# Performance work log

Hardware: AMD Instinct MI355X
Metric: run time of the kernel (lower is better)

The kernel has to match this reference:

```python
import jax, jax.numpy as jnp
import numpy as np
import math

B, S, D, H, DH = 1, 2048, 2048, 16, 64  # batch, seq, d_model, n_heads, d_head
LAMBDA_INIT = 0.8
EPS = 1e-5


def setup_inputs() -> dict:
    key = jax.random.key(0)
    ks = jax.random.split(key, 10)
    w_scale = 0.02
    inner = 2 * DH * H  # == D here
    return {
        "x": jax.random.normal(ks[0], (B, S, D), dtype=jnp.float32),
        "Wq": jax.random.normal(ks[1], (D, inner), dtype=jnp.float32) * w_scale,
        "Wk": jax.random.normal(ks[2], (D, inner), dtype=jnp.float32) * w_scale,
        "Wv": jax.random.normal(ks[3], (D, inner), dtype=jnp.float32) * w_scale,
        "Wo": jax.random.normal(ks[4], (inner, D), dtype=jnp.float32) * w_scale,
        "lambda_q1": jax.random.normal(ks[5], (DH,), dtype=jnp.float32) * 0.1,
        "lambda_k1": jax.random.normal(ks[6], (DH,), dtype=jnp.float32) * 0.1,
        "lambda_q2": jax.random.normal(ks[7], (DH,), dtype=jnp.float32) * 0.1,
        "lambda_k2": jax.random.normal(ks[8], (DH,), dtype=jnp.float32) * 0.1,
        "gn_weight": jnp.ones((inner,), dtype=jnp.float32),
        "gn_bias": jnp.zeros((inner,), dtype=jnp.float32),
    }


def reference(x, Wq, Wk, Wv, Wo, lambda_q1, lambda_k1, lambda_q2, lambda_k2,
              gn_weight, gn_bias):
    b, s, _ = x.shape
    dh = lambda_q1.shape[0]
    h = Wq.shape[1] // (2 * dh)
    scale = 1.0 / math.sqrt(dh)

    q = (x @ Wq).reshape(b, s, h, 2, dh)
    k = (x @ Wk).reshape(b, s, h, 2, dh)
    v = (x @ Wv).reshape(b, s, h, 2 * dh)

    # [B,H,S,dh]
    q1 = jnp.swapaxes(q[..., 0, :], 1, 2)
    q2 = jnp.swapaxes(q[..., 1, :], 1, 2)
    k1 = jnp.swapaxes(k[..., 0, :], 1, 2)
    k2 = jnp.swapaxes(k[..., 1, :], 1, 2)
    vh = jnp.swapaxes(v, 1, 2)  # [B,H,S,2*dh]

    score1 = jnp.einsum("bhsd,bhtd->bhst", q1, k1) * scale
    score2 = jnp.einsum("bhsd,bhtd->bhst", q2, k2) * scale
    attn1 = jax.nn.softmax(score1, axis=-1)
    attn2 = jax.nn.softmax(score2, axis=-1)

    lam = (jnp.exp(jnp.sum(lambda_q1 * lambda_k1))
           - jnp.exp(jnp.sum(lambda_q2 * lambda_k2)) + LAMBDA_INIT)

    out = jnp.einsum("bhst,bhtd->bhsd", attn1 - lam * attn2, vh)  # [B,H,S,2dh]
    out = jnp.swapaxes(out, 1, 2)  # [B,S,H,2dh]

    # GroupNorm: n_heads groups over the channel dim, per token
    mu = jnp.mean(out, axis=-1, keepdims=True)
    var = jnp.var(out, axis=-1, keepdims=True)
    out = (out - mu) * jax.lax.rsqrt(var + EPS)
    gw = gn_weight.reshape(h, 2 * dh)
    gb = gn_bias.reshape(h, 2 * dh)
    out = out * gw + gb

    out = out * (1.0 - LAMBDA_INIT)
    return out.reshape(b, s, -1) @ Wo
```

## Files before the change

### kernel.cpp

```cpp
#include <hip/hip_runtime.h>
#include <hip/hip_bf16.h>

typedef unsigned short u16;
typedef __attribute__((ext_vector_type(8))) short short8;
typedef __attribute__((ext_vector_type(4))) short short4v;
typedef __attribute__((ext_vector_type(4))) float f32x4;

#define S_DIM 2048
#define D_DIM 2048
#define H_NUM 16
#define DH_NUM 64

__device__ __forceinline__ u16 f2bf(float f) {
    union { float f; unsigned u; } x; x.f = f;
    unsigned r = x.u + 0x7fff + ((x.u >> 16) & 1);
    return (u16)(r >> 16);
}

__device__ __forceinline__ void gload16(const void* g, void* l) {
    __builtin_amdgcn_global_load_lds(
        (const __attribute__((address_space(1))) unsigned int*)g,
        (__attribute__((address_space(3))) unsigned int*)l, 16, 0, 0);
}

__device__ __forceinline__ void transpose_body(const float* __restrict__ src,
                                               u16* __restrict__ dst,
                                               int tx, int ty, int t)
{
    __shared__ float tile[64][65];
    const int r0 = ty * 64, c0 = tx * 64;
#pragma unroll
    for (int p = 0; p < 4; ++p) {
        int r = p * 16 + (t >> 4), c = (t & 15) * 4;
        float4 v = *(const float4*)&src[(long)(r0 + r) * D_DIM + c0 + c];
        tile[r][c] = v.x; tile[r][c + 1] = v.y;
        tile[r][c + 2] = v.z; tile[r][c + 3] = v.w;
    }
    __syncthreads();
#pragma unroll
    for (int p = 0; p < 2; ++p) {
        int ch = t + p * 256;
        int i = ch >> 3, j0 = (ch & 7) * 8;
        short8 o;
#pragma unroll
        for (int jj = 0; jj < 8; ++jj)
            o[jj] = (short)f2bf(tile[j0 + jj][i]);
        *(short8*)&dst[(long)(c0 + i) * D_DIM + r0 + j0] = o;
    }
}

__global__ __launch_bounds__(256)
void transpose_fast(const float* __restrict__ src, u16* __restrict__ dst)
{
    transpose_body(src, dst, blockIdx.x, blockIdx.y, threadIdx.x);
}

__global__ __launch_bounds__(256)
void prep4(const float* __restrict__ x,
           const float* __restrict__ Wq, const float* __restrict__ Wk,
           const float* __restrict__ Wv,
           u16* __restrict__ XB, u16* T0, u16* T1, u16* T2)
{
    const int z = blockIdx.z, t = threadIdx.x, bx = blockIdx.x;
    if (z == 0) {
        long i0 = ((long)bx * 256 + t) * 16;
        short8 o0, o1;
#pragma unroll
        for (int j = 0; j < 2; ++j) {
            float4 a = *(const float4*)&x[i0 + j * 8];
            float4 b = *(const float4*)&x[i0 + j * 8 + 4];
            short8& o = j ? o1 : o0;
            o[0] = (short)f2bf(a.x); o[1] = (short)f2bf(a.y);
            o[2] = (short)f2bf(a.z); o[3] = (short)f2bf(a.w);
            o[4] = (short)f2bf(b.x); o[5] = (short)f2bf(b.y);
            o[6] = (short)f2bf(b.z); o[7] = (short)f2bf(b.w);
        }
        *(short8*)&XB[i0] = o0;
        *(short8*)&XB[i0 + 8] = o1;
    } else {
        const float* src = (z == 1) ? Wq : (z == 2) ? Wk : Wv;
        u16* dst         = (z == 1) ? T0 : (z == 2) ? T1 : T2;
        transpose_body(src, dst, bx & 31, bx >> 5, t);
    }
}

__global__ __launch_bounds__(256)
void cvt_bf16(const float* __restrict__ src, u16* __restrict__ dst)
{
    int i = (blockIdx.x * 256 + threadIdx.x) * 4;
    float4 v = *(const float4*)(src + i);
    ushort4 o;
    o.x = f2bf(v.x); o.y = f2bf(v.y); o.z = f2bf(v.z); o.w = f2bf(v.w);
    *(ushort4*)(dst + i) = o;
}

__global__ __launch_bounds__(256, 2)
void gemm128(const u16* __restrict__ A,
             const u16* B0, const u16* B1, const u16* B2,
             u16* C0, u16* C1, u16* C2, int zbase)
{
    const int Kd = D_DIM, N = D_DIM, M = S_DIM;
    const int z = blockIdx.z + zbase;
    const u16* Bt = (z == 0) ? B0 : (z == 1) ? B1 : B2;
    u16* C        = (z == 0) ? C0 : (z == 1) ? C1 : C2;

    __shared__ __attribute__((aligned(16))) u16 As[128 * 32];
    __shared__ __attribute__((aligned(16))) u16 Bs[128 * 32];

    const int tid = threadIdx.x, lane = tid & 63, wave = tid >> 6;
    const int bm = blockIdx.x * 128, bn = blockIdx.y * 128;

    const int lrow = lane >> 2;
    const int gchunk = (lane & 3) ^ ((lane >> 3) & 3);
    const long aoff0 = (long)(bm + wave * 32 + lrow) * Kd + gchunk * 8;
    const long aoff1 = aoff0 + 16L * Kd;
    const long boff0 = (long)(bn + wave * 32 + lrow) * Kd + gchunk * 8;
    const long boff1 = boff0 + 16L * Kd;
    u16* as0 = &As[wave * 1024];
    u16* as1 = &As[wave * 1024 + 512];
    u16* bs0 = &Bs[wave * 1024];
    u16* bs1 = &Bs[wave * 1024 + 512];

    const int wr = (wave >> 1) * 64, wc = (wave & 1) * 64;
    const int fr = lane & 15, fq = lane >> 4;

    f32x4 acc[4][4];
    for (int i = 0; i < 4; ++i)
        for (int j = 0; j < 4; ++j) { f32x4 zz = {0.f,0.f,0.f,0.f}; acc[i][j] = zz; }

    for (int k0 = 0; k0 < Kd; k0 += 32) {
        gload16(A + aoff0 + k0, as0);
        gload16(A + aoff1 + k0, as1);
        gload16(Bt + boff0 + k0, bs0);
        gload16(Bt + boff1 + k0, bs1);
        __syncthreads();

        short8 af[4], bf[4];
#pragma unroll
        for (int i = 0; i < 4; ++i) {
            int m = wr + i * 16 + fr;
            int slot = fq ^ ((m >> 1) & 3);
            af[i] = *(const short8*)&As[m * 32 + slot * 8];
            int n = wc + i * 16 + fr;
            int slotb = fq ^ ((n >> 1) & 3);
            bf[i] = *(const short8*)&Bs[n * 32 + slotb * 8];
        }
#pragma unroll
        for (int i = 0; i < 4; ++i)
#pragma unroll
            for (int j = 0; j < 4; ++j)
                acc[i][j] = __builtin_amdgcn_mfma_f32_16x16x32_bf16(af[i], bf[j], acc[i][j], 0, 0, 0);
        __syncthreads();
    }

    const float sc = (z == 0) ? 0.125f : 1.0f;
#pragma unroll
    for (int i = 0; i < 4; ++i) {
        int row = bm + wr + i * 16 + fq * 4;
#pragma unroll
        for (int j = 0; j < 4; ++j) {
            int col = bn + wc + j * 16 + fr;
#pragma unroll
            for (int r = 0; r < 4; ++r) {
                u16 v = f2bf(acc[i][j][r] * sc);
                if (z == 2) C[(long)col * M + (row + r)] = v;
                else        C[(long)(row + r) * N + col] = v;
            }
        }
    }
}

__global__ __launch_bounds__(256, 2)
void gemm_out(const u16* __restrict__ A, const u16* __restrict__ Bt,
              float* __restrict__ C)
{
    const int Kd = D_DIM, N = D_DIM;

    __shared__ __attribute__((aligned(16))) u16 As[64 * 32];
    __shared__ __attribute__((aligned(16))) u16 Bs[128 * 32];

    const int tid = threadIdx.x, lane = tid & 63, wave = tid >> 6;
    const int bm = blockIdx.x * 64, bn = blockIdx.y * 128;

    const int lrow = lane >> 2;
    const int gchunk = (lane & 3) ^ ((lane >> 3) & 3);
    const long aoff  = (long)(bm + wave * 16 + lrow) * Kd + gchunk * 8;
    const long boff0 = (long)(bn + wave * 32 + lrow) * Kd + gchunk * 8;
    const long boff1 = boff0 + 16L * Kd;
    u16* as  = &As[wave * 512];
    u16* bs0 = &Bs[wave * 1024];
    u16* bs1 = &Bs[wave * 1024 + 512];

    const int wr = (wave >> 1) * 32, wc = (wave & 1) * 64;
    const int fr = lane & 15, fq = lane >> 4;

    f32x4 acc[2][4];
    for (int i = 0; i < 2; ++i)
        for (int j = 0; j < 4; ++j) { f32x4 zz = {0.f,0.f,0.f,0.f}; acc[i][j] = zz; }

    for (int k0 = 0; k0 < Kd; k0 += 32) {
        gload16(A + aoff + k0, as);
        gload16(Bt + boff0 + k0, bs0);
        gload16(Bt + boff1 + k0, bs1);
        __syncthreads();

        short8 af[2], bf[4];
#pragma unroll
        for (int i = 0; i < 2; ++i) {
            int m = wr + i * 16 + fr;
            int slot = fq ^ ((m >> 1) & 3);
            af[i] = *(const short8*)&As[m * 32 + slot * 8];
        }
#pragma unroll
        for (int j = 0; j < 4; ++j) {
            int n = wc + j * 16 + fr;
            int slotb = fq ^ ((n >> 1) & 3);
            bf[j] = *(const short8*)&Bs[n * 32 + slotb * 8];
        }
#pragma unroll
        for (int i = 0; i < 2; ++i)
#pragma unroll
            for (int j = 0; j < 4; ++j)
                acc[i][j] = __builtin_amdgcn_mfma_f32_16x16x32_bf16(af[i], bf[j], acc[i][j], 0, 0, 0);
        __syncthreads();
    }

#pragma unroll
    for (int i = 0; i < 2; ++i) {
        int row = bm + wr + i * 16 + fq * 4;
#pragma unroll
        for (int j = 0; j < 4; ++j) {
            int col = bn + wc + j * 16 + fr;
#pragma unroll
            for (int r = 0; r < 4; ++r)
                C[(long)(row + r) * N + col] = acc[i][j][r];
        }
    }
}

__global__ __launch_bounds__(256, 2)
void diff_attn(const u16* __restrict__ Qm, const u16* __restrict__ Km,
               const u16* __restrict__ Vt,
               const float* __restrict__ lq1, const float* __restrict__ lk1,
               const float* __restrict__ lq2, const float* __restrict__ lk2,
               const float* __restrict__ gw, const float* __restrict__ gb,
               u16* __restrict__ Y)
{
    __shared__ __attribute__((aligned(16))) u16 K1s[2][64 * 72];
    __shared__ __attribute__((aligned(16))) u16 K2s[2][64 * 72];
    __shared__ __attribute__((aligned(16))) u16 Vts[2][128 * 72];

    const int tid = threadIdx.x, lane = tid & 63, wave = tid >> 6;
    const int h = blockIdx.y;
    const int q0 = blockIdx.x * 64 + wave * 16;
    const int fr = lane & 15, qq = lane >> 4;

    float d1 = 0.f, d2 = 0.f;
    for (int i = 0; i < DH_NUM; ++i) {
        d1 += lq1[i] * lk1[i];
        d2 += lq2[i] * lk2[i];
    }
    const float lam = __expf(d1) - __expf(d2) + 0.8f;

    short8 q1f[2], q2f[2];
    {
        const u16* qb = Qm + (long)(q0 + fr) * D_DIM + h * 128;
        q1f[0] = *(const short8*)(qb + qq * 8);
        q1f[1] = *(const short8*)(qb + 32 + qq * 8);
        q2f[0] = *(const short8*)(qb + 64 + qq * 8);
        q2f[1] = *(const short8*)(qb + 96 + qq * 8);
    }

    f32x4 a1[8], a2[8];
    for (int n = 0; n < 8; ++n) { f32x4 zz = {0.f,0.f,0.f,0.f}; a1[n] = zz; a2[n] = zz; }
    float ls1 = 0.f, ls2 = 0.f;

    const int t0 = tid >> 3, c0 = tid & 7;
    short8 k1r[2], k2r[2], vr[4];

    auto load_tile = [&](int kb) {
        const long krow = (long)(kb * 64) * D_DIM + h * 128;
        k1r[0] = *(const short8*)&Km[krow + (long)t0 * D_DIM + c0 * 8];
        k2r[0] = *(const short8*)&Km[krow + (long)t0 * D_DIM + 64 + c0 * 8];
        k1r[1] = *(const short8*)&Km[krow + (long)(t0 + 32) * D_DIM + c0 * 8];
        k2r[1] = *(const short8*)&Km[krow + (long)(t0 + 32) * D_DIM + 64 + c0 * 8];
#pragma unroll
        for (int it = 0; it < 4; ++it)
            vr[it] = *(const short8*)&Vt[(long)(h * 128 + t0 + it * 32) * S_DIM + kb * 64 + c0 * 8];
    };
    auto store_tile = [&](int b) {
        *(short8*)&K1s[b][t0 * 72 + c0 * 8] = k1r[0];
        *(short8*)&K2s[b][t0 * 72 + c0 * 8] = k2r[0];
        *(short8*)&K1s[b][(t0 + 32) * 72 + c0 * 8] = k1r[1];
        *(short8*)&K2s[b][(t0 + 32) * 72 + c0 * 8] = k2r[1];
#pragma unroll
        for (int it = 0; it < 4; ++it)
            *(short8*)&Vts[b][(t0 + it * 32) * 72 + c0 * 8] = vr[it];
    };

    load_tile(0);
    store_tile(0);
    int p = 0;

    for (int kb = 0; kb < S_DIM / 64; ++kb) {
        __syncthreads();
        const bool more = (kb + 1 < S_DIM / 64);
        if (more) load_tile(kb + 1);

#pragma unroll
        for (int j = 0; j < 4; ++j) {
            f32x4 s1 = {0.f,0.f,0.f,0.f}, s2 = {0.f,0.f,0.f,0.f};
#pragma unroll
            for (int ks = 0; ks < 2; ++ks) {
                short8 k1 = *(const short8*)&K1s[p][(j * 16 + fr) * 72 + ks * 32 + qq * 8];
                short8 k2 = *(const short8*)&K2s[p][(j * 16 + fr) * 72 + ks * 32 + qq * 8];
                s1 = __builtin_amdgcn_mfma_f32_16x16x32_bf16(k1, q1f[ks], s1, 0, 0, 0);
                s2 = __builtin_amdgcn_mfma_f32_16x16x32_bf16(k2, q2f[ks], s2, 0, 0, 0);
            }
            short4v p1, p2;
#pragma unroll
            for (int r = 0; r < 4; ++r) {
                float e1 = __expf(s1[r]);
                float e2 = __expf(s2[r]);
                ls1 += e1; ls2 += e2;
                p1[r] = (short)f2bf(e1);
                p2[r] = (short)f2bf(e2);
            }
#pragma unroll
            for (int n = 0; n < 8; ++n) {
                short4v vf = *(const short4v*)&Vts[p][(n * 16 + fr) * 72 + j * 16 + qq * 4];
                a1[n] = __builtin_amdgcn_mfma_f32_16x16x16bf16_1k(vf, p1, a1[n], 0, 0, 0);
                a2[n] = __builtin_amdgcn_mfma_f32_16x16x16bf16_1k(vf, p2, a2[n], 0, 0, 0);
            }
        }

        if (more) store_tile(p ^ 1);
        p ^= 1;
    }

    float L1 = ls1, L2 = ls2;
    L1 += __shfl_xor(L1, 16, 64); L1 += __shfl_xor(L1, 32, 64);
    L2 += __shfl_xor(L2, 16, 64); L2 += __shfl_xor(L2, 32, 64);
    const float i1 = 1.f / L1, i2 = lam / L2;

    float o[8][4], sum = 0.f, sq = 0.f;
#pragma unroll
    for (int n = 0; n < 8; ++n)
#pragma unroll
        for (int r = 0; r < 4; ++r) {
            float v = a1[n][r] * i1 - a2[n][r] * i2;
            o[n][r] = v; sum += v; sq += v * v;
        }
    sum += __shfl_xor(sum, 16, 64); sum += __shfl_xor(sum, 32, 64);
    sq  += __shfl_xor(sq, 16, 64);  sq  += __shfl_xor(sq, 32, 64);
    const float mean = sum * (1.f / 128.f);
    const float var = sq * (1.f / 128.f) - mean * mean;
    const float inv = rsqrtf(var + 1e-5f);

    const long yrow = (long)(q0 + fr) * D_DIM + h * 128;
#pragma unroll
    for (int n = 0; n < 8; ++n) {
        float4 g4 = *(const float4*)&gw[h * 128 + n * 16 + qq * 4];
        float4 b4 = *(const float4*)&gb[h * 128 + n * 16 + qq * 4];
        ushort4 st;
        st.x = f2bf(((o[n][0] - mean) * inv * g4.x + b4.x) * 0.2f);
        st.y = f2bf(((o[n][1] - mean) * inv * g4.y + b4.y) * 0.2f);
        st.z = f2bf(((o[n][2] - mean) * inv * g4.z + b4.z) * 0.2f);
        st.w = f2bf(((o[n][3] - mean) * inv * g4.w + b4.w) * 0.2f);
        *(ushort4*)&Y[yrow + n * 16 + qq * 4] = st;
    }
}

extern "C" void kernel_launch(void* const* d_in, const int* in_sizes, int n_in,
                              void* d_out, int out_size, void* d_ws, size_t ws_size,
                              hipStream_t stream)
{
    const float* x   = (const float*)d_in[0];
    const float* Wq  = (const float*)d_in[1];
    const float* Wk  = (const float*)d_in[2];
    const float* Wv  = (const float*)d_in[3];
    const float* Wo  = (const float*)d_in[4];
    const float* lq1 = (const float*)d_in[5];
    const float* lk1 = (const float*)d_in[6];
    const float* lq2 = (const float*)d_in[7];
    const float* lk2 = (const float*)d_in[8];
    const float* gw  = (const float*)d_in[9];
    const float* gb  = (const float*)d_in[10];

    char* ws = (char*)d_ws;
    const size_t SEG = (size_t)D_DIM * D_DIM * sizeof(u16);
    const dim3 tgrid(32, 32), agrid(32, 16), ogrid(32, 16);

    if (ws_size >= 7 * SEG) {
        u16* XB  = (u16*)(ws + 0 * SEG);
        u16* WTq = (u16*)(ws + 1 * SEG);
        u16* WTk = (u16*)(ws + 2 * SEG);
        u16* WTv = (u16*)(ws + 3 * SEG);
        u16* Qb  = (u16*)(ws + 4 * SEG);
        u16* Kb  = (u16*)(ws + 5 * SEG);
        u16* Vt  = (u16*)(ws + 6 * SEG);
        u16* WTo = WTq;
        u16* Yb  = WTk;

        prep4<<<dim3(1024, 1, 4), 256, 0, stream>>>(x, Wq, Wk, Wv,
                                                    XB, WTq, WTk, WTv);
        gemm128<<<dim3(16, 16, 3), 256, 0, stream>>>(XB, WTq, WTk, WTv,
                                                     Qb, Kb, Vt, 0);
        transpose_fast<<<tgrid, 256, 0, stream>>>(Wo, WTo);
        diff_attn<<<agrid, 256, 0, stream>>>(Qb, Kb, Vt, lq1, lk1, lq2, lk2,
                                             gw, gb, Yb);
        gemm_out<<<ogrid, 256, 0, stream>>>(Yb, WTo, (float*)d_out);
    } else {
        u16* XB = (u16*)(ws + 0 * SEG);
        u16* WT = (u16*)(ws + 1 * SEG);
        u16* Qb = (u16*)(ws + 2 * SEG);
        u16* Kb = (u16*)(ws + 3 * SEG);
        u16* Vt = (u16*)(ws + 4 * SEG);

        cvt_bf16<<<4096, 256, 0, stream>>>(x, XB);
        transpose_fast<<<tgrid, 256, 0, stream>>>(Wq, WT);
        gemm128<<<dim3(16, 16, 1), 256, 0, stream>>>(XB, WT, WT, WT, Qb, Qb, Qb, 0);
        transpose_fast<<<tgrid, 256, 0, stream>>>(Wk, WT);
        gemm128<<<dim3(16, 16, 1), 256, 0, stream>>>(XB, WT, WT, WT, Kb, Kb, Kb, 1);
        transpose_fast<<<tgrid, 256, 0, stream>>>(Wv, WT);
        gemm128<<<dim3(16, 16, 1), 256, 0, stream>>>(XB, WT, WT, WT, Vt, Vt, Vt, 2);
        diff_attn<<<agrid, 256, 0, stream>>>(Qb, Kb, Vt, lq1, lk1, lq2, lk2,
                                             gw, gb, XB);
        transpose_fast<<<tgrid, 256, 0, stream>>>(Wo, WT);
        gemm_out<<<ogrid, 256, 0, stream>>>(XB, WT, (float*)d_out);
    }
}
```

Before: 313.9 us.

## Double-buffer GEMM tiles via registers, use exp2 with prescaled Q, packed bf16 converts

```diff
diff --git a/kernel.cpp b/kernel.cpp
--- a/kernel.cpp
+++ b/kernel.cpp
@@ -11,16 +11,23 @@
 #define H_NUM 16
 #define DH_NUM 64
 
+#if __has_builtin(__builtin_amdgcn_exp2f)
+#define EXP2(x) __builtin_amdgcn_exp2f(x)
+#else
+#define EXP2(x) exp2f(x)
+#endif
+
 __device__ __forceinline__ u16 f2bf(float f) {
     union { float f; unsigned u; } x; x.f = f;
     unsigned r = x.u + 0x7fff + ((x.u >> 16) & 1);
     return (u16)(r >> 16);
 }
 
-__device__ __forceinline__ void gload16(const void* g, void* l) {
-    __builtin_amdgcn_global_load_lds(
-        (const __attribute__((address_space(1))) unsigned int*)g,
-        (__attribute__((address_space(3))) unsigned int*)l, 16, 0, 0);
+__device__ __forceinline__ unsigned pk_bf16(float a, float b) {
+    union { __hip_bfloat162 h; unsigned u; } cv;
+    float2 t; t.x = a; t.y = b;
+    cv.h = __float22bfloat162_rn(t);
+    return cv.u;
 }
 
 __device__ __forceinline__ void transpose_body(const float* __restrict__ src,
@@ -104,8 +111,8 @@
     const u16* Bt = (z == 0) ? B0 : (z == 1) ? B1 : B2;
     u16* C        = (z == 0) ? C0 : (z == 1) ? C1 : C2;
 
-    __shared__ __attribute__((aligned(16))) u16 As[128 * 32];
-    __shared__ __attribute__((aligned(16))) u16 Bs[128 * 32];
+    __shared__ __attribute__((aligned(16))) u16 As[2][128 * 32];
+    __shared__ __attribute__((aligned(16))) u16 Bs[2][128 * 32];
 
     const int tid = threadIdx.x, lane = tid & 63, wave = tid >> 6;
     const int bm = blockIdx.x * 128, bn = blockIdx.y * 128;
@@ -116,55 +123,89 @@
     const long aoff1 = aoff0 + 16L * Kd;
     const long boff0 = (long)(bn + wave * 32 + lrow) * Kd + gchunk * 8;
     const long boff1 = boff0 + 16L * Kd;
-    u16* as0 = &As[wave * 1024];
-    u16* as1 = &As[wave * 1024 + 512];
-    u16* bs0 = &Bs[wave * 1024];
-    u16* bs1 = &Bs[wave * 1024 + 512];
+    const int ldst = wave * 1024 + lane * 8;
 
     const int wr = (wave >> 1) * 64, wc = (wave & 1) * 64;
     const int fr = lane & 15, fq = lane >> 4;
+
+    short8 rA0, rA1, rB0, rB1;
+    auto load_t = [&](int k0) {
+        rA0 = *(const short8*)(A + aoff0 + k0);
+        rA1 = *(const short8*)(A + aoff1 + k0);
+        rB0 = *(const short8*)(Bt + boff0 + k0);
+        rB1 = *(const short8*)(Bt + boff1 + k0);
+    };
+    auto store_t = [&](int b) {
+        *(short8*)&As[b][ldst] = rA0;
+        *(short8*)&As[b][ldst + 512] = rA1;
+        *(short8*)&Bs[b][ldst] = rB0;
+        *(short8*)&Bs[b][ldst + 512] = rB1;
+    };
 
     f32x4 acc[4][4];
     for (int i = 0; i < 4; ++i)
         for (int j = 0; j < 4; ++j) { f32x4 zz = {0.f,0.f,0.f,0.f}; acc[i][j] = zz; }
 
+    load_t(0);
+    store_t(0);
+    int p = 0;
+
     for (int k0 = 0; k0 < Kd; k0 += 32) {
-        gload16(A + aoff0 + k0, as0);
-        gload16(A + aoff1 + k0, as1);
-        gload16(Bt + boff0 + k0, bs0);
-        gload16(Bt + boff1 + k0, bs1);
         __syncthreads();
+        const bool more = (k0 + 32 < Kd);
+        if (more) load_t(k0 + 32);
 
         short8 af[4], bf[4];
 #pragma unroll
         for (int i = 0; i < 4; ++i) {
             int m = wr + i * 16 + fr;
             int slot = fq ^ ((m >> 1) & 3);
-            af[i] = *(const short8*)&As[m * 32 + slot * 8];
+            af[i] = *(const short8*)&As[p][m * 32 + slot * 8];
             int n = wc + i * 16 + fr;
             int slotb = fq ^ ((n >> 1) & 3);
-            bf[i] = *(const short8*)&Bs[n * 32 + slotb * 8];
-        }
-#pragma unroll
-        for (int i = 0; i < 4; ++i)
-#pragma unroll
-            for (int j = 0; j < 4; ++j)
-                acc[i][j] = __builtin_amdgcn_mfma_f32_16x16x32_bf16(af[i], bf[j], acc[i][j], 0, 0, 0);
-        __syncthreads();
-    }
-
-    const float sc = (z == 0) ? 0.125f : 1.0f;
-#pragma unroll
-    for (int i = 0; i < 4; ++i) {
-        int row = bm + wr + i * 16 + fq * 4;
-#pragma unroll
-        for (int j = 0; j < 4; ++j) {
-            int col = bn + wc + j * 16 + fr;
-#pragma unroll
-            for (int r = 0; r < 4; ++r) {
-                u16 v = f2bf(acc[i][j][r] * sc);
-                if (z == 2) C[(long)col * M + (row + r)] = v;
-                else        C[(long)(row + r) * N + col] = v;
+            bf[i] = *(const short8*)&Bs[p][n * 32 + slotb * 8];
+        }
+        if (z == 2) {
+#pragma unroll
+            for (int i = 0; i < 4; ++i)
+#pragma unroll
+                for (int j = 0; j < 4; ++j)
+                    acc[i][j] = __builtin_amdgcn_mfma_f32_16x16x32_bf16(bf[j], af[i], acc[i][j], 0, 0, 0);
+        } else {
+#pragma unroll
+            for (int i = 0; i < 4; ++i)
+#pragma unroll
+                for (int j = 0; j < 4; ++j)
+                    acc[i][j] = __builtin_amdgcn_mfma_f32_16x16x32_bf16(af[i], bf[j], acc[i][j], 0, 0, 0);
+        }
+
+        if (more) store_t(p ^ 1);
+        p ^= 1;
+    }
+
+    if (z == 2) {
+#pragma unroll
+        for (int i = 0; i < 4; ++i) {
+            int tok = bm + wr + i * 16 + fr;
+#pragma unroll
+            for (int j = 0; j < 4; ++j) {
+                int ch = bn + wc + j * 16 + fq * 4;
+#pragma unroll
+                for (int r = 0; r < 4; ++r)
+                    C[(long)(ch + r) * M + tok] = f2bf(acc[i][j][r]);
+            }
+        }
+    } else {
+        const float sc = (z == 0) ? 0.125f * 1.44269504f : 1.0f;
+#pragma unroll
+        for (int i = 0; i < 4; ++i) {
+            int row = bm + wr + i * 16 + fq * 4;
+#pragma unroll
+            for (int j = 0; j < 4; ++j) {
+                int col = bn + wc + j * 16 + fr;
+#pragma unroll
+                for (int r = 0; r < 4; ++r)
+                    C[(long)(row + r) * N + col] = f2bf(acc[i][j][r] * sc);
             }
         }
     }
@@ -176,8 +217,8 @@
 {
     const int Kd = D_DIM, N = D_DIM;
 
-    __shared__ __attribute__((aligned(16))) u16 As[64 * 32];
-    __shared__ __attribute__((aligned(16))) u16 Bs[128 * 32];
+    __shared__ __attribute__((aligned(16))) u16 As[2][64 * 32];
+    __shared__ __attribute__((aligned(16))) u16 Bs[2][128 * 32];
 
     const int tid = threadIdx.x, lane = tid & 63, wave = tid >> 6;
     const int bm = blockIdx.x * 64, bn = blockIdx.y * 128;
@@ -187,42 +228,58 @@
     const long aoff  = (long)(bm + wave * 16 + lrow) * Kd + gchunk * 8;
     const long boff0 = (long)(bn + wave * 32 + lrow) * Kd + gchunk * 8;
     const long boff1 = boff0 + 16L * Kd;
-    u16* as  = &As[wave * 512];
-    u16* bs0 = &Bs[wave * 1024];
-    u16* bs1 = &Bs[wave * 1024 + 512];
+    const int lA = wave * 512 + lane * 8;
+    const int lB = wave * 1024 + lane * 8;
 
     const int wr = (wave >> 1) * 32, wc = (wave & 1) * 64;
     const int fr = lane & 15, fq = lane >> 4;
+
+    short8 rA, rB0, rB1;
+    auto load_t = [&](int k0) {
+        rA  = *(const short8*)(A + aoff + k0);
+        rB0 = *(const short8*)(Bt + boff0 + k0);
+        rB1 = *(const short8*)(Bt + boff1 + k0);
+    };
+    auto store_t = [&](int b) {
+        *(short8*)&As[b][lA] = rA;
+        *(short8*)&Bs[b][lB] = rB0;
+        *(short8*)&Bs[b][lB + 512] = rB1;
+    };
 
     f32x4 acc[2][4];
     for (int i = 0; i < 2; ++i)
         for (int j = 0; j < 4; ++j) { f32x4 zz = {0.f,0.f,0.f,0.f}; acc[i][j] = zz; }
 
+    load_t(0);
+    store_t(0);
+    int p = 0;
+
     for (int k0 = 0; k0 < Kd; k0 += 32) {
-        gload16(A + aoff + k0, as);
-        gload16(Bt + boff0 + k0, bs0);
-        gload16(Bt + boff1 + k0, bs1);
         __syncthreads();
+        const bool more = (k0 + 32 < Kd);
+        if (more) load_t(k0 + 32);
 
         short8 af[2], bf[4];
 #pragma unroll
         for (int i = 0; i < 2; ++i) {
             int m = wr + i * 16 + fr;
             int slot = fq ^ ((m >> 1) & 3);
-            af[i] = *(const short8*)&As[m * 32 + slot * 8];
+            af[i] = *(const short8*)&As[p][m * 32 + slot * 8];
         }
 #pragma unroll
         for (int j = 0; j < 4; ++j) {
             int n = wc + j * 16 + fr;
             int slotb = fq ^ ((n >> 1) & 3);
-            bf[j] = *(const short8*)&Bs[n * 32 + slotb * 8];
+            bf[j] = *(const short8*)&Bs[p][n * 32 + slotb * 8];
         }
 #pragma unroll
         for (int i = 0; i < 2; ++i)
 #pragma unroll
             for (int j = 0; j < 4; ++j)
                 acc[i][j] = __builtin_amdgcn_mfma_f32_16x16x32_bf16(af[i], bf[j], acc[i][j], 0, 0, 0);
-        __syncthreads();
+
+        if (more) store_t(p ^ 1);
+        p ^= 1;
     }
 
 #pragma unroll
@@ -317,20 +374,21 @@
                 s1 = __builtin_amdgcn_mfma_f32_16x16x32_bf16(k1, q1f[ks], s1, 0, 0, 0);
                 s2 = __builtin_amdgcn_mfma_f32_16x16x32_bf16(k2, q2f[ks], s2, 0, 0, 0);
             }
-            short4v p1, p2;
+            float e1[4], e2[4];
 #pragma unroll
             for (int r = 0; r < 4; ++r) {
-                float e1 = __expf(s1[r]);
-                float e2 = __expf(s2[r]);
-                ls1 += e1; ls2 += e2;
-                p1[r] = (short)f2bf(e1);
-                p2[r] = (short)f2bf(e2);
+                e1[r] = EXP2(s1[r]);
+                e2[r] = EXP2(s2[r]);
+                ls1 += e1[r]; ls2 += e2[r];
             }
+            union { short4v s; unsigned u[2]; } P1, P2;
+            P1.u[0] = pk_bf16(e1[0], e1[1]); P1.u[1] = pk_bf16(e1[2], e1[3]);
+            P2.u[0] = pk_bf16(e2[0], e2[1]); P2.u[1] = pk_bf16(e2[2], e2[3]);
 #pragma unroll
             for (int n = 0; n < 8; ++n) {
                 short4v vf = *(const short4v*)&Vts[p][(n * 16 + fr) * 72 + j * 16 + qq * 4];
-                a1[n] = __builtin_amdgcn_mfma_f32_16x16x16bf16_1k(vf, p1, a1[n], 0, 0, 0);
-                a2[n] = __builtin_amdgcn_mfma_f32_16x16x16bf16_1k(vf, p2, a2[n], 0, 0, 0);
+                a1[n] = __builtin_amdgcn_mfma_f32_16x16x16bf16_1k(vf, P1.s, a1[n], 0, 0, 0);
+                a2[n] = __builtin_amdgcn_mfma_f32_16x16x16bf16_1k(vf, P2.s, a2[n], 0, 0, 0);
             }
         }
 
```

After: 333.9 us. +6.4%, slower.
